# Optimization experiments

Measured on AMD Instinct MI355X. Metric: run time of the kernel, lower is better.

Reference implementation:

```python
import jax, jax.numpy as jnp
import numpy as np

N_OPCODES = 31
B, S, D = 64, 16, 1024
MAX_STEPS = 16


def setup_inputs() -> dict:
    key = jax.random.key(0)
    k1, k2, k3, k4 = jax.random.split(key, 4)
    return {
        "opcode_logits": jax.random.normal(k1, (B, S, N_OPCODES), dtype=jnp.float32),
        "operands": jax.random.normal(k2, (B, S, 4), dtype=jnp.float32),
        "signal": jax.random.normal(k3, (B, D), dtype=jnp.float32),
        "op_kernels": jax.random.normal(k4, (N_OPCODES, D, D), dtype=jnp.float32) * 0.01,
    }


def reference(opcode_logits, operands, signal, op_kernels):
    # opcode_logits: (B,S,O), operands: (B,S,4), signal: (B,D), op_kernels: (O,D,D)
    n_steps = min(opcode_logits.shape[1], MAX_STEPS)
    weights = jax.nn.softmax(opcode_logits, axis=-1)  # (B,S,O)

    # time-major inputs for scan: (n_steps, B, O) and (n_steps, B, 1)
    ws = jnp.swapaxes(weights[:, :n_steps], 0, 1)
    gate_logits = jnp.swapaxes(operands[:, :n_steps, 3:4], 0, 1)

    def step(h, inputs):
        w, gl = inputs  # (B,O), (B,1)
        gate = jax.nn.sigmoid(gl)
        # equivalent to h @ (sum_o w_o K_o) but never forms the (B,D,D) kernel
        transformed = jnp.einsum('bo,bd,odk->bk', w, h, op_kernels)
        h_new = gate * transformed + (1.0 - gate) * h
        return h_new, None

    h, _ = jax.lax.scan(step, signal, (ws, gate_logits))
    return h
```

## Files before the change

### kernel.cpp

```cpp
#include <hip/hip_runtime.h>
#include <cstddef>
#include <cstdint>

#define NB 64
#define ND 1024
#define NO 31
#define NSTEPS 16
#define KS 124
#define KT32 992
#define KC32 8

typedef _Float16 half8 __attribute__((ext_vector_type(8)));
typedef float floatx4 __attribute__((ext_vector_type(4)));

__global__ void softmax_k(const float* __restrict__ logits, float* __restrict__ W) {
    int row = blockIdx.x * blockDim.x + threadIdx.x;
    if (row >= NB * NSTEPS) return;
    const float* x = logits + (size_t)row * NO;
    float m = -1e30f;
    for (int o = 0; o < NO; ++o) m = fmaxf(m, x[o]);
    float e[NO]; float s = 0.f;
    for (int o = 0; o < NO; ++o) { e[o] = expf(x[o] - m); s += e[o]; }
    float inv = 1.0f / s;
    float* wo = W + (size_t)row * NO;
    for (int o = 0; o < NO; ++o) wo[o] = e[o] * inv;
}

__global__ void kconv_k(const float* __restrict__ K, _Float16* __restrict__ Ktf) {
    int gid = blockIdx.x * 256 + threadIdx.x;
    int l  = gid & 63;
    int kt = (gid >> 6) % KT32;
    int ns = gid / (64 * KT32);
    int kbase = kt * 32 + (l >> 4) * 8;
    int n  = ns * 16 + (l & 15);
    int o  = kbase >> 10;
    int d0 = kbase & 1023;
    const float* src = K + ((size_t)o << 20) + (size_t)d0 * ND + n;
    half8 v;
    #pragma unroll
    for (int j = 0; j < 8; ++j) v[j] = (_Float16)src[(size_t)j * ND];
    *(half8*)(Ktf + (size_t)gid * 8) = v;
}

__global__ __launch_bounds__(256, 4) void gemm_k(
    const float* __restrict__ h, const _Float16* __restrict__ Ktf,
    const float* __restrict__ W, float* __restrict__ P, int step)
{
    __shared__ _Float16 lds_a[64 * 256];
    int nb = blockIdx.x;
    int ks = blockIdx.y;
    int tid = threadIdx.x;
    int l = tid & 63, w = tid >> 6;
    int o = ks >> 2;
    int d_base = (ks & 3) * 256;

    {
        int b = tid >> 2, u = tid & 3;
        float wv = W[((size_t)b * NSTEPS + step) * NO + o];
        const float* hb = h + (size_t)b * ND + d_base;
        #pragma unroll
        for (int li = 0; li < 8; ++li) {
            int p = li * 4 + u;
            float4 x0 = *(const float4*)(hb + p * 8);
            float4 x1 = *(const float4*)(hb + p * 8 + 4);
            half8 v;
            v[0] = (_Float16)(x0.x * wv); v[1] = (_Float16)(x0.y * wv);
            v[2] = (_Float16)(x0.z * wv); v[3] = (_Float16)(x0.w * wv);
            v[4] = (_Float16)(x1.x * wv); v[5] = (_Float16)(x1.y * wv);
            v[6] = (_Float16)(x1.z * wv); v[7] = (_Float16)(x1.w * wv);
            *(half8*)&lds_a[(size_t)(p * 64 + b) * 8] = v;
        }
    }
    __syncthreads();

    int ml = l & 15, q = l >> 4;
    int ns0 = nb * 8 + w * 2;
    const half8* Bp0 = (const half8*)Ktf + ((size_t)ns0 * KT32 + (size_t)ks * KC32) * 64 + l;
    const half8* Bp1 = Bp0 + (size_t)KT32 * 64;
    const half8* Ap  = (const half8*)lds_a;

    floatx4 acc[2][4] = {};

#define LOADB(n0, n1, S) half8 n0 = Bp0[(S) * 64]; half8 n1 = Bp1[(S) * 64];
    LOADB(b00, b01, 0) LOADB(b10, b11, 1) LOADB(b20, b21, 2) LOADB(b30, b31, 3)
    LOADB(b40, b41, 4) LOADB(b50, b51, 5) LOADB(b60, b61, 6) LOADB(b70, b71, 7)
#undef LOADB

#define STEP(n0, n1, S) { \
    int abase = ((S) * 4 + q) * 64 + ml; \
    half8 a0 = Ap[abase]; \
    half8 a1 = Ap[abase + 16]; \
    half8 a2 = Ap[abase + 32]; \
    half8 a3 = Ap[abase + 48]; \
    acc[0][0] = __builtin_amdgcn_mfma_f32_16x16x32_f16(a0, n0, acc[0][0], 0, 0, 0); \
    acc[0][1] = __builtin_amdgcn_mfma_f32_16x16x32_f16(a1, n0, acc[0][1], 0, 0, 0); \
    acc[0][2] = __builtin_amdgcn_mfma_f32_16x16x32_f16(a2, n0, acc[0][2], 0, 0, 0); \
    acc[0][3] = __builtin_amdgcn_mfma_f32_16x16x32_f16(a3, n0, acc[0][3], 0, 0, 0); \
    acc[1][0] = __builtin_amdgcn_mfma_f32_16x16x32_f16(a0, n1, acc[1][0], 0, 0, 0); \
    acc[1][1] = __builtin_amdgcn_mfma_f32_16x16x32_f16(a1, n1, acc[1][1], 0, 0, 0); \
    acc[1][2] = __builtin_amdgcn_mfma_f32_16x16x32_f16(a2, n1, acc[1][2], 0, 0, 0); \
    acc[1][3] = __builtin_amdgcn_mfma_f32_16x16x32_f16(a3, n1, acc[1][3], 0, 0, 0); \
    }
    STEP(b00, b01, 0) STEP(b10, b11, 1) STEP(b20, b21, 2) STEP(b30, b31, 3)
    STEP(b40, b41, 4) STEP(b50, b51, 5) STEP(b60, b61, 6) STEP(b70, b71, 7)
#undef STEP

    float* Pks = P + (size_t)ks * (NB * ND);
    #pragma unroll
    for (int nsub = 0; nsub < 2; ++nsub) {
        int n = (ns0 + nsub) * 16 + ml;
        #pragma unroll
        for (int mt = 0; mt < 4; ++mt) {
            #pragma unroll
            for (int r = 0; r < 4; ++r) {
                int b = mt * 16 + q * 4 + r;
                Pks[(size_t)b * ND + n] = acc[nsub][mt][r];
            }
        }
    }
}

__global__ void update_k(const float* __restrict__ hin, const float* __restrict__ P,
                         const float* __restrict__ operands, float* __restrict__ hout,
                         int step)
{
    __shared__ float red[256];
    int tid = threadIdx.x;
    int w = tid >> 6, o = tid & 63;
    int gbase = blockIdx.x * 64;
    int g = gbase + o;
    const float* p = P + (size_t)(w * 31) * (NB * ND) + g;
    float s = 0.f;
    #pragma unroll
    for (int i = 0; i < 31; ++i) s += p[(size_t)i * (NB * ND)];
    red[tid] = s;
    __syncthreads();
    if (tid < 64) {
        float tot = red[tid] + red[tid + 64] + red[tid + 128] + red[tid + 192];
        int b = g >> 10;
        float gl = operands[((size_t)b * NSTEPS + step) * 4 + 3];
        float gt = 1.0f / (1.0f + expf(-gl));
        hout[g] = gt * tot + (1.0f - gt) * hin[g];
    }
}

extern "C" void kernel_launch(void* const* d_in, const int* in_sizes, int n_in,
                              void* d_out, int out_size, void* d_ws, size_t ws_size,
                              hipStream_t stream)
{
    const float* logits   = (const float*)d_in[0];
    const float* operands = (const float*)d_in[1];
    const float* signal   = (const float*)d_in[2];
    const float* opk      = (const float*)d_in[3];
    float* out = (float*)d_out;
    char* ws = (char*)d_ws;

    size_t offW = 0;
    size_t offP = 131072;
    size_t offH = offP + (size_t)KS * NB * ND * 4;
    size_t offK = offH + 2ull * NB * ND * 4;

    float*    W  = (float*)(ws + offW);
    float*    P  = (float*)(ws + offP);
    float*    h0 = (float*)(ws + offH);
    float*    h1 = h0 + NB * ND;
    _Float16* Ktf = (_Float16*)(ws + offK);

    softmax_k<<<dim3(4), 256, 0, stream>>>(logits, W);
    kconv_k<<<dim3(15872), 256, 0, stream>>>(opk, Ktf);

    const float* hc = signal;
    float* hn = h0;
    for (int t = 0; t < NSTEPS; ++t) {
        gemm_k<<<dim3(8, KS), 256, 0, stream>>>(hc, Ktf, W, P, t);
        float* dst = (t == NSTEPS - 1) ? out : hn;
        update_k<<<dim3(1024), 256, 0, stream>>>(hc, P, operands, dst, t);
        hc = dst;
        hn = (hn == h0) ? h1 : h0;
    }
}
```

Before: 592.2 us.

## Transpose kernel weights via swizzled LDS tile and widen GEMM N-tile per wave

The fp32-to-fp16 weight conversion now stages a 32x256 tile in shared memory with an XOR swizzle. Global reads become coalesced float4 loads instead of strided scalar reads down columns. The per-step GEMM gives each wave 4 N-subtiles instead of 2 and halves the grid in N, so each A fragment read from LDS is reused across more MFMAs. The cost is more registers for B (32 half8) and accumulators (16 floatx4), which may lower occupancy, plus fewer blocks per step.

```diff
diff --git a/kernel.cpp b/kernel.cpp
--- a/kernel.cpp
+++ b/kernel.cpp
@@ -26,23 +26,44 @@
     for (int o = 0; o < NO; ++o) wo[o] = e[o] * inv;
 }
 
-__global__ void kconv_k(const float* __restrict__ K, _Float16* __restrict__ Ktf) {
-    int gid = blockIdx.x * 256 + threadIdx.x;
-    int l  = gid & 63;
-    int kt = (gid >> 6) % KT32;
-    int ns = gid / (64 * KT32);
-    int kbase = kt * 32 + (l >> 4) * 8;
-    int n  = ns * 16 + (l & 15);
-    int o  = kbase >> 10;
-    int d0 = kbase & 1023;
-    const float* src = K + ((size_t)o << 20) + (size_t)d0 * ND + n;
-    half8 v;
-    #pragma unroll
-    for (int j = 0; j < 8; ++j) v[j] = (_Float16)src[(size_t)j * ND];
-    *(half8*)(Ktf + (size_t)gid * 8) = v;
-}
-
-__global__ __launch_bounds__(256, 4) void gemm_k(
+__global__ __launch_bounds__(256) void kconv_k(const float* __restrict__ K,
+                                               _Float16* __restrict__ Ktf) {
+    __shared__ float tile[32 * 256];
+    int kt  = blockIdx.x >> 2;
+    int nb4 = blockIdx.x & 3;
+    int tid = threadIdx.x;
+    int lane = tid & 63, w = tid >> 6;
+
+    {
+        const float* src = K + ((size_t)kt * 32) * ND + nb4 * 256;
+        #pragma unroll
+        for (int i = 0; i < 8; ++i) {
+            int r = i * 4 + w;
+            int x = lane * 4;
+            int xs = x ^ (((r >> 3) & 1) << 4);
+            float4 v = *(const float4*)(src + (size_t)r * ND + x);
+            *(float4*)&tile[r * 256 + xs] = v;
+        }
+    }
+    __syncthreads();
+
+    int kl0 = (lane >> 4) * 8;
+    int swz = ((lane >> 4) & 1) << 4;
+    #pragma unroll
+    for (int i = 0; i < 4; ++i) {
+        int ns_local = i * 4 + w;
+        int nl = ns_local * 16 + (lane & 15);
+        int xsw = nl ^ swz;
+        half8 v;
+        #pragma unroll
+        for (int j = 0; j < 8; ++j) v[j] = (_Float16)tile[(kl0 + j) * 256 + xsw];
+        int ns = nb4 * 16 + ns_local;
+        size_t unit = ((size_t)ns * KT32 + kt) * 64 + lane;
+        *(half8*)(Ktf + unit * 8) = v;
+    }
+}
+
+__global__ __launch_bounds__(256) void gemm_k(
     const float* __restrict__ h, const _Float16* __restrict__ Ktf,
     const float* __restrict__ W, float* __restrict__ P, int step)
 {
@@ -74,47 +95,45 @@
     __syncthreads();
 
     int ml = l & 15, q = l >> 4;
-    int ns0 = nb * 8 + w * 2;
-    const half8* Bp0 = (const half8*)Ktf + ((size_t)ns0 * KT32 + (size_t)ks * KC32) * 64 + l;
-    const half8* Bp1 = Bp0 + (size_t)KT32 * 64;
-    const half8* Ap  = (const half8*)lds_a;
-
-    floatx4 acc[2][4] = {};
-
-#define LOADB(n0, n1, S) half8 n0 = Bp0[(S) * 64]; half8 n1 = Bp1[(S) * 64];
-    LOADB(b00, b01, 0) LOADB(b10, b11, 1) LOADB(b20, b21, 2) LOADB(b30, b31, 3)
-    LOADB(b40, b41, 4) LOADB(b50, b51, 5) LOADB(b60, b61, 6) LOADB(b70, b71, 7)
-#undef LOADB
-
-#define STEP(n0, n1, S) { \
-    int abase = ((S) * 4 + q) * 64 + ml; \
-    half8 a0 = Ap[abase]; \
-    half8 a1 = Ap[abase + 16]; \
-    half8 a2 = Ap[abase + 32]; \
-    half8 a3 = Ap[abase + 48]; \
-    acc[0][0] = __builtin_amdgcn_mfma_f32_16x16x32_f16(a0, n0, acc[0][0], 0, 0, 0); \
-    acc[0][1] = __builtin_amdgcn_mfma_f32_16x16x32_f16(a1, n0, acc[0][1], 0, 0, 0); \
-    acc[0][2] = __builtin_amdgcn_mfma_f32_16x16x32_f16(a2, n0, acc[0][2], 0, 0, 0); \
-    acc[0][3] = __builtin_amdgcn_mfma_f32_16x16x32_f16(a3, n0, acc[0][3], 0, 0, 0); \
-    acc[1][0] = __builtin_amdgcn_mfma_f32_16x16x32_f16(a0, n1, acc[1][0], 0, 0, 0); \
-    acc[1][1] = __builtin_amdgcn_mfma_f32_16x16x32_f16(a1, n1, acc[1][1], 0, 0, 0); \
-    acc[1][2] = __builtin_amdgcn_mfma_f32_16x16x32_f16(a2, n1, acc[1][2], 0, 0, 0); \
-    acc[1][3] = __builtin_amdgcn_mfma_f32_16x16x32_f16(a3, n1, acc[1][3], 0, 0, 0); \
-    }
-    STEP(b00, b01, 0) STEP(b10, b11, 1) STEP(b20, b21, 2) STEP(b30, b31, 3)
-    STEP(b40, b41, 4) STEP(b50, b51, 5) STEP(b60, b61, 6) STEP(b70, b71, 7)
-#undef STEP
+    int ns0 = nb * 16 + w * 4;
+    const half8* Ap = (const half8*)lds_a;
+
+    half8 breg[4][8];
+    #pragma unroll
+    for (int t = 0; t < 4; ++t) {
+        const half8* bp = (const half8*)Ktf
+            + ((size_t)(ns0 + t) * KT32 + (size_t)ks * KC32) * 64 + l;
+        #pragma unroll
+        for (int s = 0; s < 8; ++s) breg[t][s] = bp[(size_t)s * 64];
+    }
+
+    floatx4 acc[4][4] = {};
+    #pragma unroll
+    for (int s = 0; s < 8; ++s) {
+        int abase = (s * 4 + q) * 64 + ml;
+        half8 a0 = Ap[abase];
+        half8 a1 = Ap[abase + 16];
+        half8 a2 = Ap[abase + 32];
+        half8 a3 = Ap[abase + 48];
+        #pragma unroll
+        for (int t = 0; t < 4; ++t) {
+            acc[t][0] = __builtin_amdgcn_mfma_f32_16x16x32_f16(a0, breg[t][s], acc[t][0], 0, 0, 0);
+            acc[t][1] = __builtin_amdgcn_mfma_f32_16x16x32_f16(a1, breg[t][s], acc[t][1], 0, 0, 0);
+            acc[t][2] = __builtin_amdgcn_mfma_f32_16x16x32_f16(a2, breg[t][s], acc[t][2], 0, 0, 0);
+            acc[t][3] = __builtin_amdgcn_mfma_f32_16x16x32_f16(a3, breg[t][s], acc[t][3], 0, 0, 0);
+        }
+    }
 
     float* Pks = P + (size_t)ks * (NB * ND);
     #pragma unroll
-    for (int nsub = 0; nsub < 2; ++nsub) {
-        int n = (ns0 + nsub) * 16 + ml;
+    for (int t = 0; t < 4; ++t) {
+        int n = (ns0 + t) * 16 + ml;
         #pragma unroll
         for (int mt = 0; mt < 4; ++mt) {
             #pragma unroll
             for (int r = 0; r < 4; ++r) {
                 int b = mt * 16 + q * 4 + r;
-                Pks[(size_t)b * ND + n] = acc[nsub][mt][r];
+                Pks[(size_t)b * ND + n] = acc[t][mt][r];
             }
         }
     }
@@ -167,12 +186,12 @@
     _Float16* Ktf = (_Float16*)(ws + offK);
 
     softmax_k<<<dim3(4), 256, 0, stream>>>(logits, W);
-    kconv_k<<<dim3(15872), 256, 0, stream>>>(opk, Ktf);
+    kconv_k<<<dim3(3968), 256, 0, stream>>>(opk, Ktf);
 
     const float* hc = signal;
     float* hn = h0;
     for (int t = 0; t < NSTEPS; ++t) {
-        gemm_k<<<dim3(8, KS), 256, 0, stream>>>(hc, Ktf, W, P, t);
+        gemm_k<<<dim3(4, KS), 256, 0, stream>>>(hc, Ktf, W, P, t);
         float* dst = (t == NSTEPS - 1) ? out : hn;
         update_k<<<dim3(1024), 256, 0, stream>>>(hc, P, operands, dst, t);
         hc = dst;
```

Result: no change. 586.0 us (-1.0%).
